# Kernel optimization log

Hardware: AMD Instinct MI355X
Metric: run time of the kernel (lower is better)

The kernel has to match this reference:

```python
import jax, jax.numpy as jnp
import numpy as np

STATE = 16
DT_RANK = 48
INNER = 1536
LN_EPS = 1e-5


def setup_inputs() -> dict:
    key = jax.random.key(0)
    ks = jax.random.split(key, 10)
    B, C, H, W = 128, 2048, 24, 12
    hid = 768
    inp = {}
    inp["x"] = jax.random.normal(ks[0], (B, C, H, W), jnp.float32)
    inp["pe_w"] = jax.random.normal(ks[1], (C, hid), jnp.float32) * 0.02
    inp["pe_b"] = jnp.zeros((hid,), jnp.float32)
    inp["ln_g"] = jnp.ones((hid,), jnp.float32)
    inp["ln_b"] = jnp.zeros((hid,), jnp.float32)
    inp["in_w"] = jax.random.normal(ks[2], (hid, 2 * INNER), jnp.float32) * 0.02
    inp["conv_w"] = jax.random.normal(ks[3], (INNER, 1, 3), jnp.float32) * 0.1
    inp["conv_b"] = jnp.zeros((INNER,), jnp.float32)
    # faithful init: A = repeat(arange(1, state+1)), A_log = log(A)
    inp["A_log"] = jnp.log(jnp.broadcast_to(jnp.arange(1, STATE + 1, dtype=jnp.float32), (INNER, STATE)))
    inp["xproj_w"] = jax.random.normal(ks[4], (INNER, DT_RANK + 2 * STATE), jnp.float32) * 0.02
    inp["dtproj_w"] = jax.random.normal(ks[5], (DT_RANK, INNER), jnp.float32) * 0.02
    inp["dtproj_b"] = jnp.zeros((INNER,), jnp.float32)
    inp["D_param"] = jnp.ones((INNER,), jnp.float32)
    inp["out_w"] = jax.random.normal(ks[6], (INNER, C), jnp.float32) * 0.02
    return inp


def _forward(x, pe_w, pe_b, ln_g, ln_b, in_w, conv_w, conv_b, A_log,
             xproj_w, dtproj_w, dtproj_b, D_param, out_w):
    B, C, H, W = x.shape
    # Patch_Embedding: AdaptiveAvgPool2d((3,3)) -- H,W divisible by 3 -> block mean
    xp = x.reshape(B, C, 3, H // 3, 3, W // 3).mean(axis=(3, 5))  # [B,C,3,3]
    tok = xp.reshape(B, C, 9).transpose(0, 2, 1)                   # [B,9,C]
    tok = tok @ pe_w + pe_b                                        # [B,9,hid]

    # Mamba: LayerNorm (biased variance)
    mu = tok.mean(-1, keepdims=True)
    var = tok.var(-1, keepdims=True)
    h = (tok - mu) / jnp.sqrt(var + LN_EPS) * ln_g + ln_b

    xz = h @ in_w                                                  # [B,9,2*inner]
    xs, z = xz[..., :INNER], xz[..., INNER:]

    # depthwise conv1d, kernel 3, pad 1
    xc = jax.lax.conv_general_dilated(
        xs.transpose(0, 2, 1), conv_w, window_strides=(1,), padding=[(1, 1)],
        feature_group_count=INNER, dimension_numbers=("NCH", "OIH", "NCH"))
    xc = (xc + conv_b[None, :, None]).transpose(0, 2, 1)           # [B,9,inner]
    xc = jax.nn.silu(xc)

    # SSM selective scan
    A = -jnp.exp(A_log)                                            # [inner,state]
    dbc = xc @ xproj_w                                             # [B,9,dtr+2*state]
    d_r = dbc[..., :DT_RANK]
    Bp = dbc[..., DT_RANK:DT_RANK + STATE]                         # [B,9,state]
    Cp = dbc[..., DT_RANK + STATE:]                                # [B,9,state]
    delta = jax.nn.softplus(d_r @ dtproj_w + dtproj_b)             # [B,9,inner]

    dA = jnp.exp(delta[..., None] * A)                             # [B,9,inner,state]
    dBu = delta[..., None] * Bp[:, :, None, :] * xc[..., None]     # [B,9,inner,state]

    def step(s, t):
        dA_i, dBu_i, C_i = t                                       # [B,inner,state],[B,inner,state],[B,state]
        s = dA_i * s + dBu_i
        y = jnp.einsum("bdn,bn->bd", s, C_i)
        return s, y

    s0 = jnp.zeros((B, INNER, STATE), xc.dtype)
    _, ys = jax.lax.scan(step, s0, (dA.transpose(1, 0, 2, 3),
                                    dBu.transpose(1, 0, 2, 3),
                                    Cp.transpose(1, 0, 2)))
    y = ys.transpose(1, 0, 2) + xc * D_param                       # [B,9,inner]

    y = y * jax.nn.silu(z)
    out = y @ out_w                                                # [B,9,C]

    # Inverse_Patch_Embedding: reshape to [B,C,3,3], bilinear upsample (align_corners=False)
    out = out.transpose(0, 2, 1).reshape(B, C, 3, 3)
    out = jax.image.resize(out, (B, C, H, W), method="bilinear")
    return out


def reference(x, pe_w, pe_b, ln_g, ln_b, in_w, conv_w, conv_b, A_log,
              xproj_w, dtproj_w, dtproj_b, D_param, out_w):
    return _forward(x, pe_w, pe_b, ln_g, ln_b, in_w, conv_w, conv_b, A_log,
                    xproj_w, dtproj_w, dtproj_b, D_param, out_w)
```

## Files before the change

kernel.cpp:

```cpp
#include <hip/hip_runtime.h>
#include <math.h>

#define Bn   128
#define Cn   2048
#define Hn   24
#define Wn   12
#define HID  768
#define NIN  1536
#define NST  16
#define DTR  48
#define Ln   9
#define Mn   (Bn*Ln)

typedef __bf16 bf16x8 __attribute__((ext_vector_type(8)));
typedef float  f32x4  __attribute__((ext_vector_type(4)));

#define GLOAD16(gsrc, ldst) \
  __builtin_amdgcn_global_load_lds((const __attribute__((address_space(1))) void*)(gsrc), \
                                   (__attribute__((address_space(3))) void*)(ldst), 16, 0, 0)

__device__ __forceinline__ unsigned short f2bf(float f) {
  unsigned u = __float_as_uint(f);
  u += 0x7fffu + ((u >> 16) & 1u);
  return (unsigned short)(u >> 16);
}
__device__ __forceinline__ float bf2f(unsigned short h) {
  return __uint_as_float(((unsigned)h) << 16);
}
__device__ __forceinline__ void split_bf(float f, unsigned short& hi, unsigned short& lo) {
  hi = f2bf(f);
  lo = f2bf(f - bf2f(hi));
}
__device__ __forceinline__ int col2(int k) { return ((k >> 5) << 6) + (k & 31); }

__global__ __launch_bounds__(256) void pool_kernel(const float* __restrict__ x,
    unsigned short* __restrict__ tok2) {
  __shared__ float4 raw[2304];
  int blk = blockIdx.x;
  int b = blk >> 6, cg = blk & 63;
  const float4* src = reinterpret_cast<const float4*>(x) + (size_t)(b * Cn + cg * 32) * 72;
  int t = threadIdx.x;
  #pragma unroll
  for (int it = 0; it < 9; ++it) raw[it * 256 + t] = src[it * 256 + t];
  __syncthreads();
  for (int cell = t; cell < 288; cell += 256) {
    int c = cell / 9, p = cell % 9, i = p / 3, j = p % 3;
    float s = 0.f;
    #pragma unroll
    for (int k = 0; k < 8; ++k) {
      float4 v = raw[c * 72 + (i * 8 + k) * 3 + j];
      s += (v.x + v.y) + (v.z + v.w);
    }
    s *= (1.0f / 32.0f);
    unsigned short hi, lo;
    split_bf(s, hi, lo);
    int cglob = cg * 32 + c;
    size_t base = ((size_t)(b * Ln + p)) * (2 * Cn) + col2(cglob);
    tok2[base] = hi; tok2[base + 32] = lo;
  }
}

__global__ __launch_bounds__(256) void tconv_kernel(const float* __restrict__ W,
    int K, int N, unsigned short* __restrict__ T2) {
  __shared__ float tile[32][33];
  int nb = blockIdx.x, kb = blockIdx.y;
  int t = threadIdx.x;
  int kl = t >> 3, n4 = (t & 7) * 4;
  float4 v = *reinterpret_cast<const float4*>(W + (size_t)(kb * 32 + kl) * N + nb * 32 + n4);
  tile[kl][n4] = v.x; tile[kl][n4 + 1] = v.y; tile[kl][n4 + 2] = v.z; tile[kl][n4 + 3] = v.w;
  __syncthreads();
  int nl = t >> 3, k4 = (t & 7) * 4;
  unsigned short hi[4], lo[4];
  #pragma unroll
  for (int i = 0; i < 4; ++i) split_bf(tile[k4 + i][nl], hi[i], lo[i]);
  size_t base = (size_t)(nb * 32 + nl) * (2 * K) + kb * 64 + k4;
  uint2 ph, pl;
  ph.x = (unsigned)hi[0] | ((unsigned)hi[1] << 16);
  ph.y = (unsigned)hi[2] | ((unsigned)hi[3] << 16);
  pl.x = (unsigned)lo[0] | ((unsigned)lo[1] << 16);
  pl.y = (unsigned)lo[2] | ((unsigned)lo[3] << 16);
  *reinterpret_cast<uint2*>(T2 + base)      = ph;
  *reinterpret_cast<uint2*>(T2 + base + 32) = pl;
}

__global__ __launch_bounds__(256) void mgemm_kernel(
    const unsigned short* __restrict__ A2, const unsigned short* __restrict__ B2,
    float* __restrict__ Cout, int M, int N, int K, int Ksub) {
  __shared__ unsigned short As[128][64];
  __shared__ unsigned short Bs[128][64];
  int t = threadIdx.x;
  int bm = blockIdx.y * 128, bn = blockIdx.x * 128;
  int wave = t >> 6, lane = t & 63;
  int wr = (wave >> 1) * 64, wc = (wave & 1) * 64;
  int lr = lane & 15, lk = lane >> 4;

  int l3 = lane >> 3, c8 = lane & 7;
  int sc = c8 ^ l3;
  size_t koff = (size_t)blockIdx.z * 2 * (size_t)Ksub;
  const unsigned short* Ab = A2 + (size_t)(bm + wave * 32 + l3) * (2 * (size_t)K) + koff + sc * 8;
  const unsigned short* Bb = B2 + (size_t)(bn + wave * 32 + l3) * (2 * (size_t)K) + koff + sc * 8;
  size_t rstep = (size_t)8 * 2 * K;
  unsigned short* AsW = &As[wave * 32][0];
  unsigned short* BsW = &Bs[wave * 32][0];

  f32x4 acc[4][4];
  #pragma unroll
  for (int m = 0; m < 4; ++m)
    #pragma unroll
    for (int n = 0; n < 4; ++n) acc[m][n] = {0.f, 0.f, 0.f, 0.f};

  for (int kk = 0; kk < Ksub; kk += 32) {
    __syncthreads();
    #pragma unroll
    for (int q = 0; q < 4; ++q) {
      GLOAD16(Ab + q * rstep + kk * 2, AsW + q * 8 * 64);
      GLOAD16(Bb + q * rstep + kk * 2, BsW + q * 8 * 64);
    }
    __syncthreads();

    bf16x8 ah[4], al[4], bh[4], bl[4];
    #pragma unroll
    for (int m = 0; m < 4; ++m) {
      int ar = wr + m * 16 + lr;
      ah[m] = *reinterpret_cast<const bf16x8*>(&As[ar][((lk    ) ^ (ar & 7)) * 8]);
      al[m] = *reinterpret_cast<const bf16x8*>(&As[ar][((4 + lk) ^ (ar & 7)) * 8]);
    }
    #pragma unroll
    for (int n = 0; n < 4; ++n) {
      int br = wc + n * 16 + lr;
      bh[n] = *reinterpret_cast<const bf16x8*>(&Bs[br][((lk    ) ^ (br & 7)) * 8]);
      bl[n] = *reinterpret_cast<const bf16x8*>(&Bs[br][((4 + lk) ^ (br & 7)) * 8]);
    }
    #pragma unroll
    for (int m = 0; m < 4; ++m)
      #pragma unroll
      for (int n = 0; n < 4; ++n) {
        acc[m][n] = __builtin_amdgcn_mfma_f32_16x16x32_bf16(ah[m], bh[n], acc[m][n], 0, 0, 0);
        acc[m][n] = __builtin_amdgcn_mfma_f32_16x16x32_bf16(ah[m], bl[n], acc[m][n], 0, 0, 0);
        acc[m][n] = __builtin_amdgcn_mfma_f32_16x16x32_bf16(al[m], bh[n], acc[m][n], 0, 0, 0);
      }
  }

  float* dst = Cout + (size_t)blockIdx.z * M * N;
  #pragma unroll
  for (int m = 0; m < 4; ++m)
    #pragma unroll
    for (int n = 0; n < 4; ++n) {
      int col = bn + wc + n * 16 + lr;
      #pragma unroll
      for (int r = 0; r < 4; ++r) {
        int row = bm + wr + m * 16 + lk * 4 + r;
        dst[(size_t)row * N + col] = acc[m][n][r];
      }
    }
}

template<int KS>
__global__ __launch_bounds__(256) void red_kernel(const float* __restrict__ part,
    float* __restrict__ out, int MN) {
  int i = blockIdx.x * 256 + threadIdx.x;
  if (i >= MN) return;
  float s = 0.f;
  #pragma unroll
  for (int ks = 0; ks < KS; ++ks) s += part[(size_t)ks * MN + i];
  out[i] = s;
}

template<int ACT>
__global__ __launch_bounds__(256) void gemm_kernel(const float* __restrict__ A, int lda,
    const float* __restrict__ Bm, const float* __restrict__ bias, float* __restrict__ Cm,
    int M, int N, int K) {
  __shared__ float As[16][68];
  __shared__ float Bs[16][68];
  int t  = threadIdx.x;
  int bm = blockIdx.y * 64, bn = blockIdx.x * 64;
  int tx = t & 15, ty = t >> 4;
  float acc[4][4] = {};
  int ar = t >> 2, ak = (t & 3) * 4;
  int br = t >> 4, bc = (t & 15) * 4;
  for (int k0 = 0; k0 < K; k0 += 16) {
    float4 av = make_float4(0.f, 0.f, 0.f, 0.f);
    if (bm + ar < M)
      av = *reinterpret_cast<const float4*>(A + (size_t)(bm + ar) * lda + k0 + ak);
    As[ak + 0][ar] = av.x; As[ak + 1][ar] = av.y;
    As[ak + 2][ar] = av.z; As[ak + 3][ar] = av.w;
    float4 bv = make_float4(0.f, 0.f, 0.f, 0.f);
    if (bn + bc < N)
      bv = *reinterpret_cast<const float4*>(Bm + (size_t)(k0 + br) * N + bn + bc);
    *reinterpret_cast<float4*>(&Bs[br][bc]) = bv;
    __syncthreads();
    #pragma unroll
    for (int kk = 0; kk < 16; ++kk) {
      float a0[4], b0[4];
      #pragma unroll
      for (int i = 0; i < 4; ++i) a0[i] = As[kk][ty * 4 + i];
      #pragma unroll
      for (int j = 0; j < 4; ++j) b0[j] = Bs[kk][tx * 4 + j];
      #pragma unroll
      for (int i = 0; i < 4; ++i)
        #pragma unroll
        for (int j = 0; j < 4; ++j)
          acc[i][j] = fmaf(a0[i], b0[j], acc[i][j]);
    }
    __syncthreads();
  }
  #pragma unroll
  for (int i = 0; i < 4; ++i) {
    int row = bm + ty * 4 + i;
    if (row >= M) continue;
    #pragma unroll
    for (int j = 0; j < 4; ++j) {
      int col = bn + tx * 4 + j;
      if (col >= N) continue;
      float v = acc[i][j];
      if (bias) v += bias[col];
      if (ACT == 1) v = fmaxf(v, 0.0f) + log1pf(expf(-fabsf(v)));
      Cm[(size_t)row * N + col] = v;
    }
  }
}

__global__ __launch_bounds__(256) void xproj_kernel(const float* __restrict__ xc,
    const float* __restrict__ w, float* __restrict__ part) {
  __shared__ float at[64][44];
  __shared__ float wt[32][80];
  int kc = blockIdx.x, mt = blockIdx.y;
  int t = threadIdx.x;
  int tx = t & 15, ty = t >> 4;
  float acc[4][5] = {};
  int sr = t >> 3, sc4 = (t & 7) * 4;
  for (int k0 = kc * 192; k0 < kc * 192 + 192; k0 += 32) {
    __syncthreads();
    float4 v0 = *reinterpret_cast<const float4*>(xc + (size_t)(mt * 64 + sr) * NIN + k0 + sc4);
    float4 v1 = *reinterpret_cast<const float4*>(xc + (size_t)(mt * 64 + sr + 32) * NIN + k0 + sc4);
    *reinterpret_cast<float4*>(&at[sr][sc4])      = v0;
    *reinterpret_cast<float4*>(&at[sr + 32][sc4]) = v1;
    for (int i = t; i < 32 * 80; i += 256)
      wt[i / 80][i % 80] = w[(size_t)(k0 + i / 80) * 80 + i % 80];
    __syncthreads();
    #pragma unroll
    for (int kk = 0; kk < 32; ++kk) {
      float a0[4], b0[5];
      #pragma unroll
      for (int i = 0; i < 4; ++i) a0[i] = at[ty * 4 + i][kk];
      #pragma unroll
      for (int j = 0; j < 5; ++j) b0[j] = wt[kk][tx + 16 * j];
      #pragma unroll
      for (int i = 0; i < 4; ++i)
        #pragma unroll
        for (int j = 0; j < 5; ++j)
          acc[i][j] = fmaf(a0[i], b0[j], acc[i][j]);
    }
  }
  #pragma unroll
  for (int i = 0; i < 4; ++i)
    #pragma unroll
    for (int j = 0; j < 5; ++j)
      part[((size_t)kc * Mn + mt * 64 + ty * 4 + i) * 80 + tx + 16 * j] = acc[i][j];
}

__global__ __launch_bounds__(256) void xpred_kernel(const float* __restrict__ part,
                                                    float* __restrict__ dbc) {
  int i = blockIdx.x * 256 + threadIdx.x;
  float s = 0.f;
  #pragma unroll
  for (int kc = 0; kc < 8; ++kc) s += part[(size_t)kc * (Mn * 80) + i];
  dbc[i] = s;
}

__global__ __launch_bounds__(256) void ln_kernel(const float* __restrict__ part1,
    const float* __restrict__ peb, const float* __restrict__ g, const float* __restrict__ be,
    unsigned short* __restrict__ h2) {
  int row = blockIdx.x;
  int t = threadIdx.x;
  float vq[3];
  #pragma unroll
  for (int q = 0; q < 3; ++q) {
    int c = t + q * 256;
    float v = peb[c];
    #pragma unroll
    for (int ks = 0; ks < 8; ++ks)
      v += part1[((size_t)ks * Mn + row) * HID + c];
    vq[q] = v;
  }
  float s  = vq[0] + vq[1] + vq[2];
  float s2 = vq[0] * vq[0] + vq[1] * vq[1] + vq[2] * vq[2];
  #pragma unroll
  for (int o = 32; o > 0; o >>= 1) {
    s  += __shfl_down(s,  o, 64);
    s2 += __shfl_down(s2, o, 64);
  }
  __shared__ float red[8];
  int wid = t >> 6, lane = t & 63;
  if (lane == 0) { red[wid] = s; red[4 + wid] = s2; }
  __syncthreads();
  float S  = red[0] + red[1] + red[2] + red[3];
  float S2 = red[4] + red[5] + red[6] + red[7];
  float mu  = S * (1.0f / HID);
  float var = S2 * (1.0f / HID) - mu * mu;
  float inv = rsqrtf(var + 1e-5f);
  #pragma unroll
  for (int q = 0; q < 3; ++q) {
    int c = t + q * 256;
    float hv = (vq[q] - mu) * inv * g[c] + be[c];
    unsigned short hi, lo;
    split_bf(hv, hi, lo);
    size_t base = (size_t)row * (2 * HID) + col2(c);
    h2[base] = hi; h2[base + 32] = lo;
  }
}

__global__ __launch_bounds__(256) void conv_silu_kernel(const float* __restrict__ xz,
    const float* __restrict__ w, const float* __restrict__ cb, float* __restrict__ xc) {
  int idx = blockIdx.x * 256 + threadIdx.x;
  if (idx >= Mn * NIN) return;
  int d  = idx % NIN;
  int bp = idx / NIN;
  int p = bp % Ln, b = bp / Ln;
  const float* base = xz + (size_t)(b * Ln) * (2 * NIN) + d;
  float acc = cb[d];
  float w0 = w[d * 3], w1 = w[d * 3 + 1], w2 = w[d * 3 + 2];
  if (p > 0)      acc += base[(size_t)(p - 1) * (2 * NIN)] * w0;
  acc += base[(size_t)p * (2 * NIN)] * w1;
  if (p < Ln - 1) acc += base[(size_t)(p + 1) * (2 * NIN)] * w2;
  float sg = 1.0f / (1.0f + expf(-acc));
  xc[idx] = acc * sg;
}

__global__ __launch_bounds__(256) void scan_kernel(const float* __restrict__ delta,
    const float* __restrict__ dbc, const float* __restrict__ xcb,
    const float* __restrict__ A_log, const float* __restrict__ Dp,
    const float* __restrict__ xz, unsigned short* __restrict__ ya2) {
  __shared__ float Bsh[Ln][NST], Csh[Ln][NST];
  int b      = blockIdx.x / (NIN / 256);
  int dchunk = blockIdx.x % (NIN / 256);
  int t = threadIdx.x;
  if (t < Ln * NST) {
    int p = t / NST, n = t % NST;
    const float* row = dbc + (size_t)(b * Ln + p) * (DTR + 2 * NST);
    Bsh[p][n] = row[DTR + n];
    Csh[p][n] = row[DTR + NST + n];
  }
  __syncthreads();
  int d = dchunk * 256 + t;
  float Ar[NST];
  #pragma unroll
  for (int n = 0; n < NST; ++n) Ar[n] = -expf(A_log[(size_t)d * NST + n]);
  float s[NST];
  #pragma unroll
  for (int n = 0; n < NST; ++n) s[n] = 0.0f;
  float Dv = Dp[d];
  int cc = col2(d);
  for (int p = 0; p < Ln; ++p) {
    size_t off = (size_t)(b * Ln + p) * NIN + d;
    float dl = delta[off];
    float u  = xcb[off];
    float du = dl * u;
    float y = 0.0f;
    #pragma unroll
    for (int n = 0; n < NST; ++n) {
      float dA = expf(dl * Ar[n]);
      s[n] = dA * s[n] + du * Bsh[p][n];
      y += s[n] * Csh[p][n];
    }
    float zv = xz[(size_t)(b * Ln + p) * (2 * NIN) + NIN + d];
    float sz = zv / (1.0f + expf(-zv));
    float yv = (y + u * Dv) * sz;
    unsigned short hi, lo;
    split_bf(yv, hi, lo);
    size_t base = (size_t)(b * Ln + p) * (2 * NIN) + cc;
    ya2[base] = hi; ya2[base + 32] = lo;
  }
}

__global__ __launch_bounds__(256) void resize_kernel(const float* __restrict__ o9,
                                                     float* __restrict__ out) {
  int idx = blockIdx.x * 256 + threadIdx.x;
  if (idx >= Bn * Cn * Hn) return;
  int y  = idx % Hn;
  int bc = idx / Hn;
  int c = bc % Cn, b = bc / Cn;
  float v[9];
  #pragma unroll
  for (int p = 0; p < 9; ++p) v[p] = o9[(size_t)(b * Ln + p) * Cn + c];
  float fy  = (y + 0.5f) * 0.125f - 0.5f;
  float fyf = floorf(fy);
  float wy  = fy - fyf;
  int y0 = (int)fyf, y1 = y0 + 1;
  y0 = min(2, max(0, y0)); y1 = min(2, max(0, y1));
  float rr[3];
  #pragma unroll
  for (int j = 0; j < 3; ++j) rr[j] = v[y0 * 3 + j] * (1.0f - wy) + v[y1 * 3 + j] * wy;
  float ov[12];
  #pragma unroll
  for (int xo = 0; xo < 12; ++xo) {
    float fx  = (xo + 0.5f) * 0.25f - 0.5f;
    float fxf = floorf(fx);
    float wx  = fx - fxf;
    int x0 = (int)fxf, x1 = x0 + 1;
    x0 = min(2, max(0, x0)); x1 = min(2, max(0, x1));
    ov[xo] = rr[x0] * (1.0f - wx) + rr[x1] * wx;
  }
  float4* op = reinterpret_cast<float4*>(out + (size_t)idx * 12);
  op[0] = make_float4(ov[0], ov[1], ov[2],  ov[3]);
  op[1] = make_float4(ov[4], ov[5], ov[6],  ov[7]);
  op[2] = make_float4(ov[8], ov[9], ov[10], ov[11]);
}

extern "C" void kernel_launch(void* const* d_in, const int* in_sizes, int n_in,
                              void* d_out, int out_size, void* d_ws, size_t ws_size,
                              hipStream_t stream) {
  const float* x        = (const float*)d_in[0];
  const float* pe_w     = (const float*)d_in[1];
  const float* pe_b     = (const float*)d_in[2];
  const float* ln_g     = (const float*)d_in[3];
  const float* ln_b     = (const float*)d_in[4];
  const float* in_w     = (const float*)d_in[5];
  const float* conv_w   = (const float*)d_in[6];
  const float* conv_b   = (const float*)d_in[7];
  const float* A_log    = (const float*)d_in[8];
  const float* xproj_w  = (const float*)d_in[9];
  const float* dtproj_w = (const float*)d_in[10];
  const float* dtproj_b = (const float*)d_in[11];
  const float* D_param  = (const float*)d_in[12];
  const float* out_w    = (const float*)d_in[13];
  float* out = (float*)d_out;
  char* ws = (char*)d_ws;

  size_t o = 0;
  auto alloc = [&](size_t bytes) { size_t r = o; o += (bytes + 255) & ~(size_t)255; return r; };
  unsigned short* tok2  = (unsigned short*)(ws + alloc((size_t)Mn * 2 * Cn * 2));
  unsigned short* peT2  = (unsigned short*)(ws + alloc((size_t)HID * 2 * Cn * 2));
  unsigned short* inT2  = (unsigned short*)(ws + alloc((size_t)2 * NIN * 2 * HID * 2));
  unsigned short* outT2 = (unsigned short*)(ws + alloc((size_t)Cn * 2 * NIN * 2));
  unsigned short* h2    = (unsigned short*)(ws + alloc((size_t)Mn * 2 * HID * 2));
  unsigned short* ya2   = (unsigned short*)(ws + alloc((size_t)Mn * 2 * NIN * 2));
  float* xz    = (float*)(ws + alloc((size_t)Mn * 2 * NIN * 4));
  float* xc    = (float*)(ws + alloc((size_t)Mn * NIN * 4));
  float* dbc   = (float*)(ws + alloc((size_t)Mn * 80 * 4));
  float* delta = (float*)(ws + alloc((size_t)Mn * NIN * 4));
  float* o9    = (float*)(ws + alloc((size_t)Mn * Cn * 4));
  float* part1 = (float*)(ws + alloc((size_t)8 * Mn * HID * 4));
  float* part2 = (float*)(ws + alloc((size_t)2 * Mn * 2 * NIN * 4));
  float* part3 = (float*)(ws + alloc((size_t)4 * Mn * Cn * 4));
  float* partx = (float*)(ws + alloc((size_t)8 * Mn * 80 * 4));

  tconv_kernel<<<dim3(HID / 32, Cn / 32), 256, 0, stream>>>(pe_w, Cn, HID, peT2);
  tconv_kernel<<<dim3(2 * NIN / 32, HID / 32), 256, 0, stream>>>(in_w, HID, 2 * NIN, inT2);
  tconv_kernel<<<dim3(Cn / 32, NIN / 32), 256, 0, stream>>>(out_w, NIN, Cn, outT2);

  pool_kernel<<<Bn * (Cn / 32), 256, 0, stream>>>(x, tok2);
  mgemm_kernel<<<dim3(HID / 128, Mn / 128, 8), 256, 0, stream>>>(
      tok2, peT2, part1, Mn, HID, Cn, Cn / 8);
  ln_kernel<<<Mn, 256, 0, stream>>>(part1, pe_b, ln_g, ln_b, h2);
  mgemm_kernel<<<dim3(2 * NIN / 128, Mn / 128, 2), 256, 0, stream>>>(
      h2, inT2, part2, Mn, 2 * NIN, HID, HID / 2);
  red_kernel<2><<<(Mn * 2 * NIN) / 256, 256, 0, stream>>>(part2, xz, Mn * 2 * NIN);
  conv_silu_kernel<<<(Mn * NIN) / 256, 256, 0, stream>>>(xz, conv_w, conv_b, xc);
  xproj_kernel<<<dim3(8, Mn / 64), 256, 0, stream>>>(xc, xproj_w, partx);
  xpred_kernel<<<(Mn * 80) / 256, 256, 0, stream>>>(partx, dbc);
  gemm_kernel<1><<<dim3(NIN / 64, Mn / 64), 256, 0, stream>>>(
      dbc, 80, dtproj_w, dtproj_b, delta, Mn, NIN, DTR);
  scan_kernel<<<Bn * (NIN / 256), 256, 0, stream>>>(
      delta, dbc, xc, A_log, D_param, xz, ya2);
  mgemm_kernel<<<dim3(Cn / 128, Mn / 128, 4), 256, 0, stream>>>(
      ya2, outT2, part3, Mn, Cn, NIN, NIN / 4);
  red_kernel<4><<<(Mn * Cn) / 256, 256, 0, stream>>>(part3, o9, Mn * Cn);
  resize_kernel<<<(Bn * Cn * Hn) / 256, 256, 0, stream>>>(o9, out);
}
```

Baseline: 364.1 us.

## Fuse split-K reductions, dt projection and softplus into consumers; merge weight transposes

```diff
diff --git a/kernel.cpp b/kernel.cpp
--- a/kernel.cpp
+++ b/kernel.cpp
@@ -35,20 +35,23 @@
 
 __global__ __launch_bounds__(256) void pool_kernel(const float* __restrict__ x,
     unsigned short* __restrict__ tok2) {
-  __shared__ float4 raw[2304];
+  __shared__ float4 raw[32][73];
   int blk = blockIdx.x;
   int b = blk >> 6, cg = blk & 63;
   const float4* src = reinterpret_cast<const float4*>(x) + (size_t)(b * Cn + cg * 32) * 72;
   int t = threadIdx.x;
   #pragma unroll
-  for (int it = 0; it < 9; ++it) raw[it * 256 + t] = src[it * 256 + t];
+  for (int it = 0; it < 9; ++it) {
+    int li = it * 256 + t;
+    raw[li / 72][li % 72] = src[li];
+  }
   __syncthreads();
   for (int cell = t; cell < 288; cell += 256) {
     int c = cell / 9, p = cell % 9, i = p / 3, j = p % 3;
     float s = 0.f;
     #pragma unroll
     for (int k = 0; k < 8; ++k) {
-      float4 v = raw[c * 72 + (i * 8 + k) * 3 + j];
+      float4 v = raw[c][(i * 8 + k) * 3 + j];
       s += (v.x + v.y) + (v.z + v.w);
     }
     s *= (1.0f / 32.0f);
@@ -60,10 +63,16 @@
   }
 }
 
-__global__ __launch_bounds__(256) void tconv_kernel(const float* __restrict__ W,
-    int K, int N, unsigned short* __restrict__ T2) {
+__global__ __launch_bounds__(256) void tconv_all_kernel(const float* __restrict__ pe_w,
+    const float* __restrict__ in_w, const float* __restrict__ out_w,
+    unsigned short* __restrict__ peT2, unsigned short* __restrict__ inT2,
+    unsigned short* __restrict__ outT2) {
   __shared__ float tile[32][33];
-  int nb = blockIdx.x, kb = blockIdx.y;
+  int bid = blockIdx.x;
+  const float* W; unsigned short* T2; int K, N, nb, kb;
+  if (bid < 1536)      { W = pe_w;  T2 = peT2;  K = Cn;  N = HID;     nb = bid % 24; kb = bid / 24; }
+  else if (bid < 3840) { int q = bid - 1536; W = in_w;  T2 = inT2;  K = HID; N = 2 * NIN; nb = q % 96; kb = q / 96; }
+  else                 { int q = bid - 3840; W = out_w; T2 = outT2; K = NIN; N = Cn;      nb = q % 64; kb = q / 64; }
   int t = threadIdx.x;
   int kl = t >> 3, n4 = (t & 7) * 4;
   float4 v = *reinterpret_cast<const float4*>(W + (size_t)(kb * 32 + kl) * N + nb * 32 + n4);
@@ -153,71 +162,6 @@
         dst[(size_t)row * N + col] = acc[m][n][r];
       }
     }
-}
-
-template<int KS>
-__global__ __launch_bounds__(256) void red_kernel(const float* __restrict__ part,
-    float* __restrict__ out, int MN) {
-  int i = blockIdx.x * 256 + threadIdx.x;
-  if (i >= MN) return;
-  float s = 0.f;
-  #pragma unroll
-  for (int ks = 0; ks < KS; ++ks) s += part[(size_t)ks * MN + i];
-  out[i] = s;
-}
-
-template<int ACT>
-__global__ __launch_bounds__(256) void gemm_kernel(const float* __restrict__ A, int lda,
-    const float* __restrict__ Bm, const float* __restrict__ bias, float* __restrict__ Cm,
-    int M, int N, int K) {
-  __shared__ float As[16][68];
-  __shared__ float Bs[16][68];
-  int t  = threadIdx.x;
-  int bm = blockIdx.y * 64, bn = blockIdx.x * 64;
-  int tx = t & 15, ty = t >> 4;
-  float acc[4][4] = {};
-  int ar = t >> 2, ak = (t & 3) * 4;
-  int br = t >> 4, bc = (t & 15) * 4;
-  for (int k0 = 0; k0 < K; k0 += 16) {
-    float4 av = make_float4(0.f, 0.f, 0.f, 0.f);
-    if (bm + ar < M)
-      av = *reinterpret_cast<const float4*>(A + (size_t)(bm + ar) * lda + k0 + ak);
-    As[ak + 0][ar] = av.x; As[ak + 1][ar] = av.y;
-    As[ak + 2][ar] = av.z; As[ak + 3][ar] = av.w;
-    float4 bv = make_float4(0.f, 0.f, 0.f, 0.f);
-    if (bn + bc < N)
-      bv = *reinterpret_cast<const float4*>(Bm + (size_t)(k0 + br) * N + bn + bc);
-    *reinterpret_cast<float4*>(&Bs[br][bc]) = bv;
-    __syncthreads();
-    #pragma unroll
-    for (int kk = 0; kk < 16; ++kk) {
-      float a0[4], b0[4];
-      #pragma unroll
-      for (int i = 0; i < 4; ++i) a0[i] = As[kk][ty * 4 + i];
-      #pragma unroll
-      for (int j = 0; j < 4; ++j) b0[j] = Bs[kk][tx * 4 + j];
-      #pragma unroll
-      for (int i = 0; i < 4; ++i)
-        #pragma unroll
-        for (int j = 0; j < 4; ++j)
-          acc[i][j] = fmaf(a0[i], b0[j], acc[i][j]);
-    }
-    __syncthreads();
-  }
-  #pragma unroll
-  for (int i = 0; i < 4; ++i) {
-    int row = bm + ty * 4 + i;
-    if (row >= M) continue;
-    #pragma unroll
-    for (int j = 0; j < 4; ++j) {
-      int col = bn + tx * 4 + j;
-      if (col >= N) continue;
-      float v = acc[i][j];
-      if (bias) v += bias[col];
-      if (ACT == 1) v = fmaxf(v, 0.0f) + log1pf(expf(-fabsf(v)));
-      Cm[(size_t)row * N + col] = v;
-    }
-  }
 }
 
 __global__ __launch_bounds__(256) void xproj_kernel(const float* __restrict__ xc,
@@ -310,34 +254,56 @@
   }
 }
 
-__global__ __launch_bounds__(256) void conv_silu_kernel(const float* __restrict__ xz,
+__global__ __launch_bounds__(256) void conv_silu_kernel(const float* __restrict__ part2,
     const float* __restrict__ w, const float* __restrict__ cb, float* __restrict__ xc) {
   int idx = blockIdx.x * 256 + threadIdx.x;
   if (idx >= Mn * NIN) return;
   int d  = idx % NIN;
   int bp = idx / NIN;
   int p = bp % Ln, b = bp / Ln;
-  const float* base = xz + (size_t)(b * Ln) * (2 * NIN) + d;
+  const float* pa = part2 + (size_t)(b * Ln) * (2 * NIN) + d;
+  const float* pb = pa + (size_t)Mn * 2 * NIN;
   float acc = cb[d];
   float w0 = w[d * 3], w1 = w[d * 3 + 1], w2 = w[d * 3 + 2];
-  if (p > 0)      acc += base[(size_t)(p - 1) * (2 * NIN)] * w0;
-  acc += base[(size_t)p * (2 * NIN)] * w1;
-  if (p < Ln - 1) acc += base[(size_t)(p + 1) * (2 * NIN)] * w2;
+  if (p > 0) {
+    size_t o1 = (size_t)(p - 1) * (2 * NIN);
+    acc += (pa[o1] + pb[o1]) * w0;
+  }
+  size_t o2 = (size_t)p * (2 * NIN);
+  acc += (pa[o2] + pb[o2]) * w1;
+  if (p < Ln - 1) {
+    size_t o3 = (size_t)(p + 1) * (2 * NIN);
+    acc += (pa[o3] + pb[o3]) * w2;
+  }
   float sg = 1.0f / (1.0f + expf(-acc));
   xc[idx] = acc * sg;
 }
 
-__global__ __launch_bounds__(256) void scan_kernel(const float* __restrict__ delta,
-    const float* __restrict__ dbc, const float* __restrict__ xcb,
-    const float* __restrict__ A_log, const float* __restrict__ Dp,
-    const float* __restrict__ xz, unsigned short* __restrict__ ya2) {
+__global__ __launch_bounds__(256) void scan_kernel(const float* __restrict__ dbc,
+    const float* __restrict__ xcb, const float* __restrict__ A_log,
+    const float* __restrict__ Dp, const float* __restrict__ part2,
+    const float* __restrict__ dtw, const float* __restrict__ dtb,
+    unsigned short* __restrict__ ya2) {
+  __shared__ float wdt[DTR * 256];
+  __shared__ float dbc9[Ln][DTR];
   __shared__ float Bsh[Ln][NST], Csh[Ln][NST];
   int b      = blockIdx.x / (NIN / 256);
   int dchunk = blockIdx.x % (NIN / 256);
   int t = threadIdx.x;
+  float4* w4 = reinterpret_cast<float4*>(wdt);
+  #pragma unroll
+  for (int it = 0; it < 12; ++it) {
+    int i4 = it * 256 + t;
+    int k = i4 >> 6, c4 = i4 & 63;
+    w4[i4] = *reinterpret_cast<const float4*>(dtw + (size_t)k * NIN + dchunk * 256 + c4 * 4);
+  }
+  for (int i = t; i < Ln * DTR; i += 256) {
+    int p = i / DTR, k = i - p * DTR;
+    dbc9[p][k] = dbc[(size_t)(b * Ln + p) * 80 + k];
+  }
   if (t < Ln * NST) {
     int p = t / NST, n = t % NST;
-    const float* row = dbc + (size_t)(b * Ln + p) * (DTR + 2 * NST);
+    const float* row = dbc + (size_t)(b * Ln + p) * 80;
     Bsh[p][n] = row[DTR + n];
     Csh[p][n] = row[DTR + NST + n];
   }
@@ -350,10 +316,16 @@
   #pragma unroll
   for (int n = 0; n < NST; ++n) s[n] = 0.0f;
   float Dv = Dp[d];
+  float bt = dtb[d];
   int cc = col2(d);
+  const float* z0 = part2 + NIN + d;
+  const float* z1 = z0 + (size_t)Mn * 2 * NIN;
   for (int p = 0; p < Ln; ++p) {
     size_t off = (size_t)(b * Ln + p) * NIN + d;
-    float dl = delta[off];
+    float a = bt;
+    #pragma unroll
+    for (int k = 0; k < DTR; ++k) a = fmaf(dbc9[p][k], wdt[k * 256 + t], a);
+    float dl = fmaxf(a, 0.0f) + log1pf(expf(-fabsf(a)));
     float u  = xcb[off];
     float du = dl * u;
     float y = 0.0f;
@@ -363,7 +335,8 @@
       s[n] = dA * s[n] + du * Bsh[p][n];
       y += s[n] * Csh[p][n];
     }
-    float zv = xz[(size_t)(b * Ln + p) * (2 * NIN) + NIN + d];
+    size_t zoff = (size_t)(b * Ln + p) * (2 * NIN);
+    float zv = z0[zoff] + z1[zoff];
     float sz = zv / (1.0f + expf(-zv));
     float yv = (y + u * Dv) * sz;
     unsigned short hi, lo;
@@ -373,38 +346,47 @@
   }
 }
 
-__global__ __launch_bounds__(256) void resize_kernel(const float* __restrict__ o9,
+__global__ __launch_bounds__(256) void resize_kernel(const float* __restrict__ part3,
                                                      float* __restrict__ out) {
-  int idx = blockIdx.x * 256 + threadIdx.x;
-  if (idx >= Bn * Cn * Hn) return;
-  int y  = idx % Hn;
-  int bc = idx / Hn;
-  int c = bc % Cn, b = bc / Cn;
-  float v[9];
-  #pragma unroll
-  for (int p = 0; p < 9; ++p) v[p] = o9[(size_t)(b * Ln + p) * Cn + c];
-  float fy  = (y + 0.5f) * 0.125f - 0.5f;
-  float fyf = floorf(fy);
-  float wy  = fy - fyf;
-  int y0 = (int)fyf, y1 = y0 + 1;
-  y0 = min(2, max(0, y0)); y1 = min(2, max(0, y1));
-  float rr[3];
-  #pragma unroll
-  for (int j = 0; j < 3; ++j) rr[j] = v[y0 * 3 + j] * (1.0f - wy) + v[y1 * 3 + j] * wy;
-  float ov[12];
-  #pragma unroll
-  for (int xo = 0; xo < 12; ++xo) {
-    float fx  = (xo + 0.5f) * 0.25f - 0.5f;
-    float fxf = floorf(fx);
-    float wx  = fx - fxf;
-    int x0 = (int)fxf, x1 = x0 + 1;
-    x0 = min(2, max(0, x0)); x1 = min(2, max(0, x1));
-    ov[xo] = rr[x0] * (1.0f - wx) + rr[x1] * wx;
-  }
-  float4* op = reinterpret_cast<float4*>(out + (size_t)idx * 12);
-  op[0] = make_float4(ov[0], ov[1], ov[2],  ov[3]);
-  op[1] = make_float4(ov[4], ov[5], ov[6],  ov[7]);
-  op[2] = make_float4(ov[8], ov[9], ov[10], ov[11]);
+  __shared__ float v[32][10];
+  int blk = blockIdx.x;
+  int b = blk >> 6, cg = blk & 63;
+  int t = threadIdx.x;
+  size_t MN3 = (size_t)Mn * Cn;
+  for (int i = t; i < 288; i += 256) {
+    int p = i >> 5, c = i & 31;
+    size_t base = (size_t)(b * Ln + p) * Cn + cg * 32 + c;
+    v[c][p] = part3[base] + part3[base + MN3] + part3[base + 2 * MN3] + part3[base + 3 * MN3];
+  }
+  __syncthreads();
+  int ch = t >> 3, sub = t & 7;
+  float* dst = out + ((size_t)b * Cn + cg * 32 + ch) * 288;
+  #pragma unroll
+  for (int q = 0; q < 9; ++q) {
+    int f = sub + q * 8;
+    int y = f / 3, xq = f - y * 3;
+    float fy  = (y + 0.5f) * 0.125f - 0.5f;
+    float fyf = floorf(fy);
+    float wy  = fy - fyf;
+    int yy = (int)fyf;
+    int y0 = min(2, max(0, yy)), y1 = min(2, max(0, yy + 1));
+    float rr[3];
+    #pragma unroll
+    for (int j = 0; j < 3; ++j)
+      rr[j] = v[ch][y0 * 3 + j] * (1.0f - wy) + v[ch][y1 * 3 + j] * wy;
+    float ov[4];
+    #pragma unroll
+    for (int xi = 0; xi < 4; ++xi) {
+      int xo = xq * 4 + xi;
+      float fx  = (xo + 0.5f) * 0.25f - 0.5f;
+      float fxf = floorf(fx);
+      float wx  = fx - fxf;
+      int xx = (int)fxf;
+      int x0 = min(2, max(0, xx)), x1 = min(2, max(0, xx + 1));
+      ov[xi] = rr[x0] * (1.0f - wx) + rr[x1] * wx;
+    }
+    *reinterpret_cast<float4*>(dst + f * 4) = make_float4(ov[0], ov[1], ov[2], ov[3]);
+  }
 }
 
 extern "C" void kernel_launch(void* const* d_in, const int* in_sizes, int n_in,
@@ -435,19 +417,14 @@
   unsigned short* outT2 = (unsigned short*)(ws + alloc((size_t)Cn * 2 * NIN * 2));
   unsigned short* h2    = (unsigned short*)(ws + alloc((size_t)Mn * 2 * HID * 2));
   unsigned short* ya2   = (unsigned short*)(ws + alloc((size_t)Mn * 2 * NIN * 2));
-  float* xz    = (float*)(ws + alloc((size_t)Mn * 2 * NIN * 4));
   float* xc    = (float*)(ws + alloc((size_t)Mn * NIN * 4));
   float* dbc   = (float*)(ws + alloc((size_t)Mn * 80 * 4));
-  float* delta = (float*)(ws + alloc((size_t)Mn * NIN * 4));
-  float* o9    = (float*)(ws + alloc((size_t)Mn * Cn * 4));
   float* part1 = (float*)(ws + alloc((size_t)8 * Mn * HID * 4));
   float* part2 = (float*)(ws + alloc((size_t)2 * Mn * 2 * NIN * 4));
   float* part3 = (float*)(ws + alloc((size_t)4 * Mn * Cn * 4));
   float* partx = (float*)(ws + alloc((size_t)8 * Mn * 80 * 4));
 
-  tconv_kernel<<<dim3(HID / 32, Cn / 32), 256, 0, stream>>>(pe_w, Cn, HID, peT2);
-  tconv_kernel<<<dim3(2 * NIN / 32, HID / 32), 256, 0, stream>>>(in_w, HID, 2 * NIN, inT2);
-  tconv_kernel<<<dim3(Cn / 32, NIN / 32), 256, 0, stream>>>(out_w, NIN, Cn, outT2);
+  tconv_all_kernel<<<6912, 256, 0, stream>>>(pe_w, in_w, out_w, peT2, inT2, outT2);
 
   pool_kernel<<<Bn * (Cn / 32), 256, 0, stream>>>(x, tok2);
   mgemm_kernel<<<dim3(HID / 128, Mn / 128, 8), 256, 0, stream>>>(
@@ -455,16 +432,12 @@
   ln_kernel<<<Mn, 256, 0, stream>>>(part1, pe_b, ln_g, ln_b, h2);
   mgemm_kernel<<<dim3(2 * NIN / 128, Mn / 128, 2), 256, 0, stream>>>(
       h2, inT2, part2, Mn, 2 * NIN, HID, HID / 2);
-  red_kernel<2><<<(Mn * 2 * NIN) / 256, 256, 0, stream>>>(part2, xz, Mn * 2 * NIN);
-  conv_silu_kernel<<<(Mn * NIN) / 256, 256, 0, stream>>>(xz, conv_w, conv_b, xc);
+  conv_silu_kernel<<<(Mn * NIN) / 256, 256, 0, stream>>>(part2, conv_w, conv_b, xc);
   xproj_kernel<<<dim3(8, Mn / 64), 256, 0, stream>>>(xc, xproj_w, partx);
   xpred_kernel<<<(Mn * 80) / 256, 256, 0, stream>>>(partx, dbc);
-  gemm_kernel<1><<<dim3(NIN / 64, Mn / 64), 256, 0, stream>>>(
-      dbc, 80, dtproj_w, dtproj_b, delta, Mn, NIN, DTR);
   scan_kernel<<<Bn * (NIN / 256), 256, 0, stream>>>(
-      delta, dbc, xc, A_log, D_param, xz, ya2);
+      dbc, xc, A_log, D_param, part2, dtproj_w, dtproj_b, ya2);
   mgemm_kernel<<<dim3(Cn / 128, Mn / 128, 4), 256, 0, stream>>>(
       ya2, outT2, part3, Mn, Cn, NIN, NIN / 4);
-  red_kernel<4><<<(Mn * Cn) / 256, 256, 0, stream>>>(part3, o9, Mn * Cn);
-  resize_kernel<<<(Bn * Cn * Hn) / 256, 256, 0, stream>>>(o9, out);
-}
+  resize_kernel<<<Bn * (Cn / 32), 256, 0, stream>>>(part3, out);
+}
```

New measurement: 324.6 us. 1.12x faster.
